# Kernel optimization log

Hardware: AMD Instinct MI355X
Metric: run time of the kernel (lower is better)

The kernel has to match this reference:

```python
import jax, jax.numpy as jnp
import numpy as np
from jax import lax

# --- module constants (from init_kwargs) ---
A_COEF = 0.7
B_COEF = 0.0
RADIUS = 8
EPS = 1e-3
EPS_LOG = 1e-6
EPS_SCALE = 1e-4
DOWN = 0.5
KSIZE = 2 * RADIUS + 1


def _sep_box_filter(x4):
    """Separable box filter on [1,1,H,W] with reflect padding (matches torch)."""
    p = jnp.pad(x4, ((0, 0), (0, 0), (RADIUS, RADIUS), (RADIUS, RADIUS)), mode='reflect')
    box_h = jnp.full((1, 1, 1, KSIZE), 1.0 / KSIZE, dtype=x4.dtype)
    box_v = jnp.full((1, 1, KSIZE, 1), 1.0 / KSIZE, dtype=x4.dtype)
    h = lax.conv(p, box_h, (1, 1), 'VALID')
    return lax.conv(h, box_v, (1, 1), 'VALID')


def _guided_filter(I2d):
    """Self-guided filter on [H,W] (guide == input)."""
    I4 = I2d[None, None]
    mean_I = _sep_box_filter(I4)
    mean_II = _sep_box_filter(I4 * I4)
    var_I = mean_II - mean_I * mean_I
    a = var_I / (var_I + EPS)
    b = mean_I - a * mean_I
    mean_a = _sep_box_filter(a)
    mean_b = _sep_box_filter(b)
    out = mean_a * I4 + mean_b
    return out[0, 0]


def _resize_bilinear(img, out_h, out_w):
    """Bilinear resize of [H,W], torch align_corners=False semantics (no antialias)."""
    in_h, in_w = img.shape
    ys = jnp.clip((jnp.arange(out_h, dtype=jnp.float32) + 0.5) * (in_h / out_h) - 0.5,
                  0.0, in_h - 1.0)
    xs = jnp.clip((jnp.arange(out_w, dtype=jnp.float32) + 0.5) * (in_w / out_w) - 0.5,
                  0.0, in_w - 1.0)
    y0 = jnp.floor(ys).astype(jnp.int32)
    x0 = jnp.floor(xs).astype(jnp.int32)
    y1 = jnp.minimum(y0 + 1, in_h - 1)
    x1 = jnp.minimum(x0 + 1, in_w - 1)
    wy = (ys - y0)[:, None]  # [out_h,1]
    wx = (xs - x0)[None, :]  # [1,out_w]
    Ia = img[y0][:, x0]
    Ib = img[y0][:, x1]
    Ic = img[y1][:, x0]
    Id = img[y1][:, x1]
    top = Ia * (1.0 - wx) + Ib * wx
    bot = Ic * (1.0 - wx) + Id * wx
    return top * (1.0 - wy) + bot * wy


def setup_inputs() -> dict:
    key = jax.random.key(0)
    x = jax.random.uniform(key, (2160, 3840, 3), dtype=jnp.float32)  # RGB in [0,1]
    return {"x": x}


def reference(x) -> jnp.ndarray:
    H, W = x.shape[0], x.shape[1]
    R, G, B = x[..., 0], x[..., 1], x[..., 2]
    Y = 0.2126 * R + 0.7152 * G + 0.0722 * B
    Y_log = jnp.log2(jnp.maximum(Y, EPS_LOG))

    # downsample -> guided filter -> upsample (DOWN < 1.0 path)
    dh, dw = int(H * DOWN), int(W * DOWN)
    Y_log_down = _resize_bilinear(Y_log, dh, dw)
    Y_base_down = _guided_filter(Y_log_down)
    Y_base = _resize_bilinear(Y_base_down, H, W)

    Y_detail = Y_log - Y_base
    Y_tm = (A_COEF * Y_base + B_COEF) + Y_detail
    Y_out = jnp.exp2(Y_tm)
    scale = Y_out / (Y + EPS_SCALE)
    out = x * scale[..., None]
    return jnp.clip(out, 0.0, 1.0)
```

## Files before the change

kernel.cpp:

```cpp
#include <hip/hip_runtime.h>

#define FH 2160
#define FW 3840
#define DH 1080
#define DW 1920
#define RAD 8
#define KS 17
#define INV_KS (1.0f / 17.0f)
#define EPS_GF 1e-3f
#define EPS_LOG 1e-6f
#define EPS_SCALE 1e-4f
#define A_COEF 0.7f

#define TS 32
#define IT 48
#define ITP 50
#define NT1 2040
#define TPX1 255

#define ATR 34
#define ATC 50
#define ATP2 52
#define BTC 34
#define BTR 18
#define BTP 35
#define NT2 4080
#define TPX2 510

__device__ __forceinline__ int refl(int p, int n) {
    p = (p < 0) ? -p : p;
    return (p >= n) ? (2 * n - 2 - p) : p;
}

__device__ __forceinline__ float luma3(float r, float g, float b) {
    return 0.2126f * r + 0.7152f * g + 0.0722f * b;
}

__global__ void __launch_bounds__(256)
k_gf_front(const float* __restrict__ x, float* __restrict__ Dg,
           float2* __restrict__ ABg) {
    __shared__ float inD[IT * ITP];
    __shared__ float2 hh[IT * TS];
    int bid = blockIdx.x;
    int swz = (bid & 7) * TPX1 + (bid >> 3);
    int bx = swz % 60, by = swz / 60;
    int tx0 = bx * TS, ty0 = by * TS;
    int t = threadIdx.x;

    for (int s = t; s < IT * IT; s += 256) {
        int li = s / IT, lj = s - li * IT;
        int gi = refl(ty0 - RAD + li, DH);
        int gj = refl(tx0 - RAD + lj, DW);
        const float* p0 = x + ((size_t)(2 * gi) * FW + (size_t)(2 * gj)) * 3;
        const float* p1 = p0 + (size_t)FW * 3;
        float2 a0 = *(const float2*)(p0);
        float2 a1 = *(const float2*)(p0 + 2);
        float2 a2 = *(const float2*)(p0 + 4);
        float2 b0 = *(const float2*)(p1);
        float2 b1 = *(const float2*)(p1 + 2);
        float2 b2 = *(const float2*)(p1 + 4);
        float y00 = fmaxf(luma3(a0.x, a0.y, a1.x), EPS_LOG);
        float y01 = fmaxf(luma3(a1.y, a2.x, a2.y), EPS_LOG);
        float y10 = fmaxf(luma3(b0.x, b0.y, b1.x), EPS_LOG);
        float y11 = fmaxf(luma3(b1.y, b2.x, b2.y), EPS_LOG);
        inD[li * ITP + lj] = 0.25f * __log2f((y00 * y01) * (y10 * y11));
    }
    __syncthreads();

    for (int task = t; task < IT * 8; task += 256) {
        int r = task >> 3, c0 = (task & 7) * 4;
        const float* row = &inD[r * ITP + c0];
        const float2* row2 = (const float2*)row;
        float s1 = 0.f, s2 = 0.f;
#pragma unroll
        for (int k = 0; k < 8; ++k) {
            float2 p = row2[k];
            s1 += p.x + p.y;
            s2 += p.x * p.x + p.y * p.y;
        }
        float v16 = row[16];
        s1 += v16; s2 += v16 * v16;
        int base = r * TS + c0;
        hh[base] = make_float2(s1 * INV_KS, s2 * INV_KS);
#pragma unroll
        for (int cc = 1; cc < 4; ++cc) {
            float vo = row[cc - 1], vi = row[cc + 16];
            s1 += vi - vo;
            s2 += vi * vi - vo * vo;
            hh[base + cc] = make_float2(s1 * INV_KS, s2 * INV_KS);
        }
    }
    __syncthreads();

    {
        int rs = t >> 5, c = t & 31;
        int r0 = rs * 4;
        float sx = 0.f, sy = 0.f;
#pragma unroll
        for (int k = 0; k < KS; ++k) {
            float2 h = hh[(r0 + k) * TS + c];
            sx += h.x; sy += h.y;
        }
#pragma unroll
        for (int rr = 0; rr < 4; ++rr) {
            int r = r0 + rr;
            if (rr > 0) {
                float2 hi = hh[(r + 16) * TS + c];
                float2 ho = hh[(r - 1) * TS + c];
                sx += hi.x - ho.x;
                sy += hi.y - ho.y;
            }
            int gi = ty0 + r;
            if (gi < DH) {
                float mI = sx * INV_KS, mII = sy * INV_KS;
                float var = mII - mI * mI;
                float av = var * __builtin_amdgcn_rcpf(var + EPS_GF);
                size_t g = (size_t)gi * DW + tx0 + c;
                ABg[g] = make_float2(av, mI - av * mI);
                Dg[g] = inD[(r + RAD) * ITP + c + RAD];
            }
        }
    }
}

__global__ void __launch_bounds__(256)
k_gf_back(const float* __restrict__ x, const float2* __restrict__ ABg,
          const float* __restrict__ Dg, float* __restrict__ out) {
    __shared__ float2 inAB[ATR * ATP2];
    __shared__ float2 hAB[ATR * BTC];
    __shared__ float baseT[BTR * BTP];
    int bid = blockIdx.x;
    int swz = (bid & 7) * TPX2 + (bid >> 3);
    int bx = swz % 60, by = swz / 60;
    int ox0 = bx * 64, oy0 = by * 32;
    int bh0 = by * 16 - 1, bw0 = bx * 32 - 1;
    int ah0 = bh0 - RAD, aw0 = bw0 - RAD;
    int t = threadIdx.x;

    if (ah0 >= 0 && ah0 + ATR <= DH && aw0 >= 0 && aw0 + ATC <= DW) {
        const float2* src = ABg + (size_t)ah0 * DW + aw0;
        for (int s = t; s < ATR * ATC; s += 256) {
            int li = s / ATC, lj = s - li * ATC;
            inAB[li * ATP2 + lj] = src[(size_t)li * DW + lj];
        }
    } else {
        for (int s = t; s < ATR * ATC; s += 256) {
            int li = s / ATC, lj = s - li * ATC;
            inAB[li * ATP2 + lj] = ABg[(size_t)refl(ah0 + li, DH) * DW + refl(aw0 + lj, DW)];
        }
    }
    __syncthreads();

    for (int task = t; task < ATR * 9; task += 256) {
        int r = task / 9, c0 = (task - r * 9) * 4;
        const float2* row = &inAB[r * ATP2 + c0];
        float s1 = 0.f, s2 = 0.f;
#pragma unroll
        for (int k = 0; k < KS; ++k) { float2 v = row[k]; s1 += v.x; s2 += v.y; }
        int base = r * BTC + c0;
#pragma unroll
        for (int cc = 0; cc < 4; ++cc) {
            if (cc > 0) {
                float2 vi = row[cc + 16], vo = row[cc - 1];
                s1 += vi.x - vo.x;
                s2 += vi.y - vo.y;
            }
            if (c0 + cc < BTC) hAB[base + cc] = make_float2(s1 * INV_KS, s2 * INV_KS);
        }
    }
    __syncthreads();

    for (int task = t; task < 5 * BTC; task += 256) {
        int rs = task / BTC, c = task - rs * BTC;
        int r0 = rs * 4;
        int sz = (rs == 4) ? 2 : 4;
        float s1 = 0.f, s2 = 0.f;
#pragma unroll
        for (int k = 0; k < KS; ++k) {
            float2 v = hAB[(r0 + k) * BTC + c];
            s1 += v.x; s2 += v.y;
        }
        for (int rr = 0; rr < sz; ++rr) {
            int r = r0 + rr;
            if (rr > 0) {
                float2 vi = hAB[(r + 16) * BTC + c];
                float2 vo = hAB[(r - 1) * BTC + c];
                s1 += vi.x - vo.x;
                s2 += vi.y - vo.y;
            }
            size_t g = (size_t)refl(bh0 + r, DH) * DW + refl(bw0 + c, DW);
            baseT[r * BTP + c] = (s1 * INV_KS) * Dg[g] + s2 * INV_KS;
        }
    }
    __syncthreads();

    for (int q = t; q < 32 * 16; q += 256) {
        int qi = q >> 4, qj = q & 15;
        int oy = oy0 + qi;
        if (oy < FH) {
            float ys = fminf(fmaxf((oy + 0.5f) * 0.5f - 0.5f, 0.f), (float)(DH - 1));
            int y0 = (int)ys;
            int y1 = min(y0 + 1, DH - 1);
            float wy = ys - (float)y0;
            const float* br0 = &baseT[(y0 - bh0) * BTP];
            const float* br1 = &baseT[(y1 - bh0) * BTP];

            size_t off = ((size_t)oy * FW + (size_t)(ox0 + 4 * qj)) * 3;
            const float4* xin = (const float4*)(x + off);
            float4 v0 = xin[0], v1 = xin[1], v2 = xin[2];
            float px[12] = {v0.x, v0.y, v0.z, v0.w, v1.x, v1.y, v1.z, v1.w,
                            v2.x, v2.y, v2.z, v2.w};
            float po[12];
#pragma unroll
            for (int p = 0; p < 4; ++p) {
                int ox = ox0 + 4 * qj + p;
                float xs = fminf(fmaxf((ox + 0.5f) * 0.5f - 0.5f, 0.f), (float)(DW - 1));
                int x0 = (int)xs;
                int x1 = min(x0 + 1, DW - 1);
                float wx = xs - (float)x0;
                int c0 = x0 - bw0, c1 = x1 - bw0;
                float top = br0[c0] * (1.f - wx) + br0[c1] * wx;
                float bot = br1[c0] * (1.f - wx) + br1[c1] * wx;
                float Yb = top * (1.f - wy) + bot * wy;

                float cr = px[3 * p], cg = px[3 * p + 1], cb = px[3 * p + 2];
                float Y = luma3(cr, cg, cb);
                float Ylog = __log2f(fmaxf(Y, EPS_LOG));
                float Yout = exp2f(A_COEF * Yb + (Ylog - Yb));
                float sc = Yout * __builtin_amdgcn_rcpf(Y + EPS_SCALE);
                po[3 * p + 0] = fminf(fmaxf(cr * sc, 0.f), 1.f);
                po[3 * p + 1] = fminf(fmaxf(cg * sc, 0.f), 1.f);
                po[3 * p + 2] = fminf(fmaxf(cb * sc, 0.f), 1.f);
            }
            float4* op = (float4*)(out + off);
            op[0] = make_float4(po[0], po[1], po[2], po[3]);
            op[1] = make_float4(po[4], po[5], po[6], po[7]);
            op[2] = make_float4(po[8], po[9], po[10], po[11]);
        }
    }
}

extern "C" void kernel_launch(void* const* d_in, const int* in_sizes, int n_in,
                              void* d_out, int out_size, void* d_ws, size_t ws_size,
                              hipStream_t stream) {
    const float* x = (const float*)d_in[0];
    float* out = (float*)d_out;
    float* ws = (float*)d_ws;
    const size_t DN = (size_t)DW * DH;

    float* D = ws;
    float2* AB = (float2*)(ws + DN);

    k_gf_front<<<dim3(NT1), dim3(256), 0, stream>>>(x, D, AB);
    k_gf_back <<<dim3(NT2), dim3(256), 0, stream>>>(x, AB, D, out);
}
```

Before: 71.40 us.

## Split back-kernel tiles per wavefront to drop block-wide barriers

The back kernel now gives each of its four wavefronts an independent 32x8 output sub-tile with private LDS buffers for the A/B box filter and base tile. The __syncthreads barriers are replaced with wave-local LDS waits, and the running-sum sliding window becomes a direct 17-tap sum per output. The grid doubles and the XCD swizzle is generalised to handle a count not divisible by 8. In exchange, each wave reloads its own halo, so redundant global A/B loads and box-filter arithmetic rise, and the direct sums cost more arithmetic than the sliding update.

Result: slower. 97.11 us (+36.0%).

```diff
diff --git a/kernel.cpp b/kernel.cpp
--- a/kernel.cpp
+++ b/kernel.cpp
@@ -18,14 +18,15 @@
 #define NT1 2040
 #define TPX1 255
 
-#define ATR 34
-#define ATC 50
-#define ATP2 52
-#define BTC 34
-#define BTR 18
-#define BTP 35
-#define NT2 4080
-#define TPX2 510
+#define W_ATR 22
+#define W_ATC 34
+#define W_HC 18
+#define W_BR 6
+#define W_BP 19
+#define W_IN (W_ATR * W_ATC * 2)
+#define W_HA (W_ATR * W_HC * 2)
+#define W_SZ 2404
+#define NT2 8100
 
 __device__ __forceinline__ int refl(int p, int n) {
     p = (p < 0) ? -p : p;
@@ -126,117 +127,107 @@
 __global__ void __launch_bounds__(256)
 k_gf_back(const float* __restrict__ x, const float2* __restrict__ ABg,
           const float* __restrict__ Dg, float* __restrict__ out) {
-    __shared__ float2 inAB[ATR * ATP2];
-    __shared__ float2 hAB[ATR * BTC];
-    __shared__ float baseT[BTR * BTP];
+    __shared__ float smem[4 * W_SZ];
     int bid = blockIdx.x;
-    int swz = (bid & 7) * TPX2 + (bid >> 3);
-    int bx = swz % 60, by = swz / 60;
-    int ox0 = bx * 64, oy0 = by * 32;
-    int bh0 = by * 16 - 1, bw0 = bx * 32 - 1;
-    int ah0 = bh0 - RAD, aw0 = bw0 - RAD;
+    int xcd = bid & 7, o8 = bid >> 3;
+    const int q = NT2 / 8, rm = NT2 % 8;
+    int wg = (xcd < rm ? xcd * (q + 1) : rm * (q + 1) + (xcd - rm) * q) + o8;
+    int bx = wg % 60, by = wg / 60;
     int t = threadIdx.x;
-
-    if (ah0 >= 0 && ah0 + ATR <= DH && aw0 >= 0 && aw0 + ATC <= DW) {
+    int w = t >> 6, lane = t & 63;
+    float* wls = smem + w * W_SZ;
+    float2* inAB = (float2*)wls;
+    float2* hAB = (float2*)(wls + W_IN);
+    float* baseT = wls + W_IN + W_HA;
+
+    int ox0 = bx * 64 + (w & 1) * 32;
+    int oy0 = by * 16 + (w >> 1) * 8;
+    int bw0 = (ox0 >> 1) - 1, bh0 = (oy0 >> 1) - 1;
+    int aw0 = bw0 - RAD, ah0 = bh0 - RAD;
+
+    if (ah0 >= 0 && ah0 + W_ATR <= DH && aw0 >= 0 && aw0 + W_ATC <= DW) {
         const float2* src = ABg + (size_t)ah0 * DW + aw0;
-        for (int s = t; s < ATR * ATC; s += 256) {
-            int li = s / ATC, lj = s - li * ATC;
-            inAB[li * ATP2 + lj] = src[(size_t)li * DW + lj];
+        for (int s = lane; s < W_ATR * W_ATC; s += 64) {
+            int r = s / W_ATC, c = s - r * W_ATC;
+            inAB[s] = src[(size_t)r * DW + c];
         }
     } else {
-        for (int s = t; s < ATR * ATC; s += 256) {
-            int li = s / ATC, lj = s - li * ATC;
-            inAB[li * ATP2 + lj] = ABg[(size_t)refl(ah0 + li, DH) * DW + refl(aw0 + lj, DW)];
-        }
-    }
-    __syncthreads();
-
-    for (int task = t; task < ATR * 9; task += 256) {
-        int r = task / 9, c0 = (task - r * 9) * 4;
-        const float2* row = &inAB[r * ATP2 + c0];
+        for (int s = lane; s < W_ATR * W_ATC; s += 64) {
+            int r = s / W_ATC, c = s - r * W_ATC;
+            inAB[s] = ABg[(size_t)refl(ah0 + r, DH) * DW + refl(aw0 + c, DW)];
+        }
+    }
+    asm volatile("s_waitcnt lgkmcnt(0)" ::: "memory");
+    __builtin_amdgcn_sched_barrier(0);
+
+    for (int s = lane; s < W_ATR * W_HC; s += 64) {
+        int r = s / W_HC, c = s - r * W_HC;
+        const float2* row = &inAB[r * W_ATC + c];
         float s1 = 0.f, s2 = 0.f;
 #pragma unroll
         for (int k = 0; k < KS; ++k) { float2 v = row[k]; s1 += v.x; s2 += v.y; }
-        int base = r * BTC + c0;
-#pragma unroll
-        for (int cc = 0; cc < 4; ++cc) {
-            if (cc > 0) {
-                float2 vi = row[cc + 16], vo = row[cc - 1];
-                s1 += vi.x - vo.x;
-                s2 += vi.y - vo.y;
-            }
-            if (c0 + cc < BTC) hAB[base + cc] = make_float2(s1 * INV_KS, s2 * INV_KS);
-        }
-    }
-    __syncthreads();
-
-    for (int task = t; task < 5 * BTC; task += 256) {
-        int rs = task / BTC, c = task - rs * BTC;
-        int r0 = rs * 4;
-        int sz = (rs == 4) ? 2 : 4;
+        hAB[s] = make_float2(s1 * INV_KS, s2 * INV_KS);
+    }
+    asm volatile("s_waitcnt lgkmcnt(0)" ::: "memory");
+    __builtin_amdgcn_sched_barrier(0);
+
+    for (int s = lane; s < W_BR * W_HC; s += 64) {
+        int r = s / W_HC, c = s - r * W_HC;
         float s1 = 0.f, s2 = 0.f;
 #pragma unroll
         for (int k = 0; k < KS; ++k) {
-            float2 v = hAB[(r0 + k) * BTC + c];
+            float2 v = hAB[(r + k) * W_HC + c];
             s1 += v.x; s2 += v.y;
         }
-        for (int rr = 0; rr < sz; ++rr) {
-            int r = r0 + rr;
-            if (rr > 0) {
-                float2 vi = hAB[(r + 16) * BTC + c];
-                float2 vo = hAB[(r - 1) * BTC + c];
-                s1 += vi.x - vo.x;
-                s2 += vi.y - vo.y;
-            }
-            size_t g = (size_t)refl(bh0 + r, DH) * DW + refl(bw0 + c, DW);
-            baseT[r * BTP + c] = (s1 * INV_KS) * Dg[g] + s2 * INV_KS;
-        }
-    }
-    __syncthreads();
-
-    for (int q = t; q < 32 * 16; q += 256) {
-        int qi = q >> 4, qj = q & 15;
+        size_t g = (size_t)refl(bh0 + r, DH) * DW + refl(bw0 + c, DW);
+        baseT[r * W_BP + c] = (s1 * INV_KS) * Dg[g] + s2 * INV_KS;
+    }
+    asm volatile("s_waitcnt lgkmcnt(0)" ::: "memory");
+    __builtin_amdgcn_sched_barrier(0);
+
+    {
+        int qi = lane >> 3, qj = lane & 7;
         int oy = oy0 + qi;
-        if (oy < FH) {
-            float ys = fminf(fmaxf((oy + 0.5f) * 0.5f - 0.5f, 0.f), (float)(DH - 1));
-            int y0 = (int)ys;
-            int y1 = min(y0 + 1, DH - 1);
-            float wy = ys - (float)y0;
-            const float* br0 = &baseT[(y0 - bh0) * BTP];
-            const float* br1 = &baseT[(y1 - bh0) * BTP];
-
-            size_t off = ((size_t)oy * FW + (size_t)(ox0 + 4 * qj)) * 3;
-            const float4* xin = (const float4*)(x + off);
-            float4 v0 = xin[0], v1 = xin[1], v2 = xin[2];
-            float px[12] = {v0.x, v0.y, v0.z, v0.w, v1.x, v1.y, v1.z, v1.w,
-                            v2.x, v2.y, v2.z, v2.w};
-            float po[12];
-#pragma unroll
-            for (int p = 0; p < 4; ++p) {
-                int ox = ox0 + 4 * qj + p;
-                float xs = fminf(fmaxf((ox + 0.5f) * 0.5f - 0.5f, 0.f), (float)(DW - 1));
-                int x0 = (int)xs;
-                int x1 = min(x0 + 1, DW - 1);
-                float wx = xs - (float)x0;
-                int c0 = x0 - bw0, c1 = x1 - bw0;
-                float top = br0[c0] * (1.f - wx) + br0[c1] * wx;
-                float bot = br1[c0] * (1.f - wx) + br1[c1] * wx;
-                float Yb = top * (1.f - wy) + bot * wy;
-
-                float cr = px[3 * p], cg = px[3 * p + 1], cb = px[3 * p + 2];
-                float Y = luma3(cr, cg, cb);
-                float Ylog = __log2f(fmaxf(Y, EPS_LOG));
-                float Yout = exp2f(A_COEF * Yb + (Ylog - Yb));
-                float sc = Yout * __builtin_amdgcn_rcpf(Y + EPS_SCALE);
-                po[3 * p + 0] = fminf(fmaxf(cr * sc, 0.f), 1.f);
-                po[3 * p + 1] = fminf(fmaxf(cg * sc, 0.f), 1.f);
-                po[3 * p + 2] = fminf(fmaxf(cb * sc, 0.f), 1.f);
-            }
-            float4* op = (float4*)(out + off);
-            op[0] = make_float4(po[0], po[1], po[2], po[3]);
-            op[1] = make_float4(po[4], po[5], po[6], po[7]);
-            op[2] = make_float4(po[8], po[9], po[10], po[11]);
-        }
+        int ox0q = ox0 + qj * 4;
+        size_t off = ((size_t)oy * FW + (size_t)ox0q) * 3;
+        const float4* xin = (const float4*)(x + off);
+        float4 v0 = xin[0], v1 = xin[1], v2 = xin[2];
+
+        float ys = fminf(fmaxf((oy + 0.5f) * 0.5f - 0.5f, 0.f), (float)(DH - 1));
+        int y0 = (int)ys;
+        int y1 = min(y0 + 1, DH - 1);
+        float wy = ys - (float)y0;
+        const float* br0 = &baseT[(y0 - bh0) * W_BP];
+        const float* br1 = &baseT[(y1 - bh0) * W_BP];
+
+        float px[12] = {v0.x, v0.y, v0.z, v0.w, v1.x, v1.y, v1.z, v1.w,
+                        v2.x, v2.y, v2.z, v2.w};
+        float po[12];
+#pragma unroll
+        for (int p = 0; p < 4; ++p) {
+            int ox = ox0q + p;
+            float xs = fminf(fmaxf((ox + 0.5f) * 0.5f - 0.5f, 0.f), (float)(DW - 1));
+            int x0 = (int)xs;
+            int x1 = min(x0 + 1, DW - 1);
+            float wx = xs - (float)x0;
+            int c0 = x0 - bw0, c1 = x1 - bw0;
+            float top = br0[c0] * (1.f - wx) + br0[c1] * wx;
+            float bot = br1[c0] * (1.f - wx) + br1[c1] * wx;
+            float Yb = top * (1.f - wy) + bot * wy;
+
+            float cr = px[3 * p], cg = px[3 * p + 1], cb = px[3 * p + 2];
+            float Y = luma3(cr, cg, cb);
+            float Ylog = __log2f(fmaxf(Y, EPS_LOG));
+            float Yout = exp2f(A_COEF * Yb + (Ylog - Yb));
+            float sc = Yout * __builtin_amdgcn_rcpf(Y + EPS_SCALE);
+            po[3 * p + 0] = fminf(fmaxf(cr * sc, 0.f), 1.f);
+            po[3 * p + 1] = fminf(fmaxf(cg * sc, 0.f), 1.f);
+            po[3 * p + 2] = fminf(fmaxf(cb * sc, 0.f), 1.f);
+        }
+        float4* op = (float4*)(out + off);
+        op[0] = make_float4(po[0], po[1], po[2], po[3]);
+        op[1] = make_float4(po[4], po[5], po[6], po[7]);
+        op[2] = make_float4(po[8], po[9], po[10], po[11]);
     }
 }
 
```
